# Kernel tuning notes

Measured on AMD Instinct MI355X. Metric: run time of the kernel, lower is better.

The kernel has to match this reference:

```python
import jax, jax.numpy as jnp
import numpy as np

B, N, K, H = 8, 1024, 16, 4
EMB = 1024

def lrelu(x):
    return jnp.where(x >= 0, x, 0.2 * x)

def bn(x, g, b):
    # eval-mode BatchNorm with running_mean=0, running_var=1
    inv = 1.0 / np.sqrt(1.0 + 1e-5)
    shape = (1, -1) + (1,) * (x.ndim - 2)
    return x * (g * inv).reshape(shape) + b.reshape(shape)

def conv1x1(x, w):
    # 1x1 conv == channel matmul; x: (B,C,...), w: (O,C)
    return jnp.einsum('bc...,oc->bo...', x, w)

def knn_idx(x, k):
    # x: (B,C,N); negative squared pairwise distance, top-k largest = nearest
    inner = -2.0 * jnp.einsum('bcn,bcm->bnm', x, x)
    xx = jnp.sum(x * x, axis=1)                      # (B,N)
    pd = -xx[:, :, None] - inner - xx[:, None, :]
    return jax.lax.top_k(pd, k)[1]                   # (B,N,k)

def graph_feature(x, idx):
    b = x.shape[0]
    xt = jnp.transpose(x, (0, 2, 1))                 # (B,N,C)
    nbr = xt[jnp.arange(b)[:, None, None], idx]      # (B,N,K,C) gather
    ctr = jnp.broadcast_to(xt[:, :, None, :], nbr.shape)
    f = jnp.concatenate([nbr - ctr, ctr], axis=-1)   # (B,N,K,2C)
    return jnp.transpose(f, (0, 3, 1, 2))            # (B,2C,N,K)

def mak(x, y, w0, g0, b0, wm, gm, bm, w1, go, bo, ws, gs, bs, out_ch, in_ch):
    # Multi-head adaptive kernel: generate per-point (out,in,H) weights from y, apply to x
    Bc, _, Nc, Kc = x.shape
    y = lrelu(bn(conv1x1(y, w0), g0, b0))
    y = lrelu(bn(conv1x1(y, wm), gm, bm))
    y = conv1x1(y, w1)                               # (B, out*in*H, N, K)
    w = jnp.transpose(y, (0, 2, 3, 1)).reshape(Bc, Nc, Kc, out_ch, in_ch, H)
    xt = jnp.transpose(x, (0, 2, 3, 1))              # (B,N,K,in)
    # per-head matmul then sum over heads == single einsum over i and h
    out = jnp.einsum('bnkoih,bnki->bonk', w, xt)
    out = bn(out, go, bo)
    idt = bn(conv1x1(x, ws), gs, bs)                 # shortcut (in != out)
    return lrelu(out + idt)


def setup_inputs() -> dict:
    ks = jax.random.split(jax.random.key(0), 48)
    it = iter(range(48))
    def nrm(shape, fan):
        return jax.random.normal(ks[next(it)], shape, jnp.float32) / np.sqrt(fan)
    def gam(c):
        return jax.random.uniform(ks[next(it)], (c,), jnp.float32, 0.5, 1.5)
    def bet(c):
        return 0.1 * jax.random.normal(ks[next(it)], (c,), jnp.float32)
    d = {}
    d['x'] = jax.random.normal(ks[next(it)], (B, 3, N), jnp.float32)
    def mak_params(p, feat_c):
        d[p + '_w0'] = nrm((64, feat_c), feat_c); d[p + '_g0'] = gam(64); d[p + '_b0'] = bet(64)
        d[p + '_wm'] = nrm((64, 64), 64); d[p + '_gm'] = gam(64); d[p + '_bm'] = bet(64)
        d[p + '_w1'] = nrm((64 * 6 * H, 64), 64)
        d[p + '_go'] = gam(64); d[p + '_bo'] = bet(64)
        d[p + '_ws'] = nrm((64, 6), 6); d[p + '_gs'] = gam(64); d[p + '_bs'] = bet(64)
    mak_params('m1', 6)
    mak_params('m2', 128)
    d['w3'] = nrm((128, 128), 128); d['g3'] = gam(128); d['b3'] = bet(128)
    d['w4'] = nrm((256, 256), 256); d['g4'] = gam(256); d['b4'] = bet(256)
    d['w5'] = nrm((EMB, 512), 512); d['g5'] = gam(EMB); d['b5'] = bet(EMB)
    d['wl1'] = nrm((512, 2 * EMB), 2 * EMB); d['bn4_g'] = gam(512); d['bn4_b'] = bet(512)
    d['wl2'] = nrm((256, 512), 512); d['bl2'] = bet(256); d['bn5_g'] = gam(256); d['bn5_b'] = bet(256)
    d['wl3'] = nrm((49, 256), 256); d['bl3'] = bet(49)
    return d


def reference(x, m1_w0, m1_g0, m1_b0, m1_wm, m1_gm, m1_bm, m1_w1, m1_go, m1_bo, m1_ws, m1_gs, m1_bs, m2_w0, m2_g0, m2_b0, m2_wm, m2_gm, m2_bm, m2_w1, m2_go, m2_bo, m2_ws, m2_gs, m2_bs, w3, g3, b3, w4, g4, b4, w5, g5, b5, wl1, bn4_g, bn4_b, wl2, bl2, bn5_g, bn5_b, wl3, bl3):
    idx = knn_idx(x, K)                              # common_idx from points
    geo = graph_feature(x, idx)                      # (B,6,N,K); feat_x == geo_x at stage 1
    h = mak(geo, geo, m1_w0, m1_g0, m1_b0, m1_wm, m1_gm, m1_bm, m1_w1, m1_go, m1_bo, m1_ws, m1_gs, m1_bs, 64, 6)
    x1 = h.max(axis=-1)                              # (B,64,N)
    feat2 = graph_feature(x1, idx)                   # (B,128,N,K)
    h = mak(geo, feat2, m2_w0, m2_g0, m2_b0, m2_wm, m2_gm, m2_bm, m2_w1, m2_go, m2_bo, m2_ws, m2_gs, m2_bs, 64, 6)
    x2 = h.max(axis=-1)                              # (B,64,N)
    x3 = lrelu(bn(conv1x1(graph_feature(x2, idx), w3), g3, b3)).max(axis=-1)   # (B,128,N)
    x4 = lrelu(bn(conv1x1(graph_feature(x3, idx), w4), g4, b4)).max(axis=-1)   # (B,256,N)
    xc = jnp.concatenate([x1, x2, x3, x4], axis=1)   # (B,512,N)
    x5 = lrelu(bn(conv1x1(xc, w5), g5, b5))          # (B,EMB,N)
    xp = jnp.concatenate([x5.max(axis=-1), x5.mean(axis=-1)], axis=1)  # (B,2*EMB)
    xf = lrelu(bn(xp @ wl1.T, bn4_g, bn4_b))
    xf = lrelu(bn(xf @ wl2.T + bl2, bn5_g, bn5_b))
    return xf @ wl3.T + bl3                           # (B,49)
```

## Files before the change

kernel.cpp:

```cpp
#include <hip/hip_runtime.h>
#include <math.h>

#define BB 8
#define NN 1024
#define KK 16
#define NKP (NN*KK)
#define BN_INV 0.99999500003749981f

typedef unsigned short u16;
typedef __attribute__((ext_vector_type(8))) short short8;
typedef __attribute__((ext_vector_type(4))) float f32x4;

#define MFMA16(a,b,c) __builtin_amdgcn_mfma_f32_16x16x32_bf16(a,b,c,0,0,0)

__device__ __forceinline__ float lrelu(float v) { return v >= 0.f ? v : 0.2f * v; }

__device__ __forceinline__ u16 f2bf(float f) {
  union { float f; unsigned u; } v; v.f = f;
  unsigned r = v.u + 0x7fff + ((v.u >> 16) & 1);
  return (u16)(r >> 16);
}
__device__ __forceinline__ float bf2f(u16 s) {
  union { unsigned u; float f; } v; v.u = ((unsigned)s) << 16;
  return v.f;
}

constexpr size_t OFF_IDX   = 0;
constexpr size_t OFF_X1P   = 524288;
constexpr size_t OFF_X2P   = 1572864;
constexpr size_t OFF_X3P   = 2621440;
constexpr size_t OFF_MUV   = 2621440;
constexpr size_t OFF_X4P   = 4718592;
constexpr size_t OFF_PMAX  = 8912896;
constexpr size_t OFF_PSUM  = 9437184;
constexpr size_t OFF_XP    = 9961472;
constexpr size_t OFF_XF1   = 10027008;
constexpr size_t OFF_XF2   = 10043392;
constexpr size_t OFF_M1WM  = 10055680;
constexpr size_t OFF_M1W1S = 10063872;
constexpr size_t OFF_M2W0S = 10117120;
constexpr size_t OFF_M2WM  = 10133504;
constexpr size_t OFF_M2W1S = 10141696;
constexpr size_t OFF_W3S   = 10194944;
constexpr size_t OFF_W4S   = 10227712;
constexpr size_t OFF_W5    = 10358784;
constexpr size_t OFF_WL1T  = 11407360;
constexpr size_t OFF_WL2T  = 15601664;
constexpr size_t OFF_WL3T  = 16125952;
constexpr size_t OFF_UV3   = 16177152;
constexpr size_t OFF_UV4   = 20371456;

struct SSeg { const float* w; const float* g; u16* dst; int O; int C; int cpl2; int ch; int stk; int start; };
struct SArgs { SSeg seg[6]; int total; };

__global__ __launch_bounds__(256) void prep_scale_bf16(SArgs a) {
  const int tid = blockIdx.x * 256 + threadIdx.x;
  if (tid >= a.total) return;
  int s = 0;
  #pragma unroll
  for (int i = 1; i < 6; ++i) if (tid >= a.seg[i].start) s = i;
  const SSeg sg = a.seg[s];
  const int e = tid - sg.start;
  const int o2 = e >> sg.cpl2;
  const int c = e & ((1 << sg.cpl2) - 1);
  float v = 0.f;
  if (sg.stk) {
    const int half = sg.O >> 1;
    const int o = o2 & (half - 1);
    const int CIN = 2 * sg.C;
    const float wd = sg.w[o * CIN + c];
    v = (o2 < half) ? wd : (sg.w[o * CIN + sg.C + c] - wd);
    v *= sg.g[o] * BN_INV;
  } else if (c < sg.C) {
    v = sg.w[o2 * sg.C + c];
    if (sg.ch && c >= sg.ch) v -= sg.w[o2 * sg.C + c - sg.ch];
    v *= sg.g[o2] * BN_INV;
  }
  sg.dst[(size_t)(c >> 5) * (sg.O * 32) + o2 * 32 + (c & 31)] = f2bf(v);
}

__global__ __launch_bounds__(256) void prep_w1s_bf16(
    const float* __restrict__ w1a, const float* __restrict__ wsa,
    const float* __restrict__ goa, const float* __restrict__ gsa,
    const float* __restrict__ w1b, const float* __restrict__ wsb,
    const float* __restrict__ gob, const float* __restrict__ gsb,
    u16* __restrict__ dsta, u16* __restrict__ dstb) {
  const int tid = blockIdx.x * 256 + threadIdx.x;
  if (tid >= 64 * 416) return;
  const float* w1 = blockIdx.y ? w1b : w1a;
  const float* wsm = blockIdx.y ? wsb : wsa;
  const float* go = blockIdx.y ? gob : goa;
  const float* gs = blockIdx.y ? gsb : gsa;
  u16* dst = blockIdx.y ? dstb : dsta;
  const int o = tid / 416, ci = tid - o * 416;
  float v = 0.f;
  if (ci < 384) {
    const int ii = ci >> 6, ch = ci & 63;
    const int base = (o * 24 + ii * 4) * 64 + ch;
    v = go[o] * BN_INV * (w1[base] + w1[base + 64] + w1[base + 128] + w1[base + 192]);
  } else if (ci < 390) {
    v = gs[o] * BN_INV * wsm[o * 6 + (ci - 384)];
  }
  dst[(size_t)(ci >> 5) * 2048 + o * 32 + (ci & 31)] = f2bf(v);
}

struct TSeg { const float* w; const float* g; float* dst; int O; int C; int start; };
struct TArgs3 { TSeg seg[3]; int total; };

__global__ __launch_bounds__(256) void prep_transpose_f32(TArgs3 a) {
  const int tid = blockIdx.x * 256 + threadIdx.x;
  if (tid >= a.total) return;
  int s = 0;
  #pragma unroll
  for (int i = 1; i < 3; ++i) if (tid >= a.seg[i].start) s = i;
  const TSeg sg = a.seg[s];
  const int e = tid - sg.start;
  const int c = e / sg.O;
  const int o = e - c * sg.O;
  float v = sg.w[o * sg.C + c];
  if (sg.g) v *= sg.g[o] * BN_INV;
  sg.dst[e] = v;
}

__global__ __launch_bounds__(256) void knn_kernel(const float* __restrict__ x, int* __restrict__ idxout) {
  const int wid  = (blockIdx.x * blockDim.x + threadIdx.x) >> 6;
  const int lane = threadIdx.x & 63;
  const int b = wid >> 10;
  const int n = wid & (NN - 1);
  const float* xb = x + b * 3 * NN;
  const float x0n = xb[n], x1n = xb[NN + n], x2n = xb[2 * NN + n];
  const float xxn = x0n * x0n + x1n * x1n + x2n * x2n;
  float pd[16];
  #pragma unroll
  for (int j = 0; j < 16; ++j) {
    const int m = j * 64 + lane;
    const float x0 = xb[m], x1 = xb[NN + m], x2 = xb[2 * NN + m];
    const float dot = x0n * x0 + x1n * x1 + x2n * x2;
    const float xxm = x0 * x0 + x1 * x1 + x2 * x2;
    pd[j] = 2.f * dot - xxn - xxm;
  }
  for (int r = 0; r < 16; ++r) {
    float bv = pd[0]; int bj = 0;
    #pragma unroll
    for (int j = 1; j < 16; ++j) if (pd[j] > bv) { bv = pd[j]; bj = j; }
    int bm = bj * 64 + lane;
    #pragma unroll
    for (int off = 32; off > 0; off >>= 1) {
      const float ov = __shfl_down(bv, off);
      const int   om = __shfl_down(bm, off);
      if (ov > bv || (ov == bv && om < bm)) { bv = ov; bm = om; }
    }
    bm = __shfl(bm, 0);
    if (lane == 0) idxout[wid * KK + r] = bm;
    const int  cj   = bm >> 6;
    const bool mine = (bm & 63) == lane;
    #pragma unroll
    for (int j = 0; j < 16; ++j) if (mine && j == cj) pd[j] = -INFINITY;
  }
}

__device__ __forceinline__ short8 bfrag64(const u16* T, int pl, int quad, int c0) {
  const int pos = ((c0 >> 3) + quad) ^ (pl & 7);
  return *(const short8*)(T + pl * 64 + pos * 8);
}
__device__ __forceinline__ void writeD64(u16* T, int pl, int quad, const f32x4 a,
                                         const float* __restrict__ bias, int obase) {
  union { ushort4 v; u16 s[4]; } pk;
  #pragma unroll
  for (int r = 0; r < 4; ++r) pk.s[r] = f2bf(lrelu(a[r] + bias[obase + quad * 4 + r]));
  const int g = (obase + quad * 4) >> 3;
  const int pos = g ^ (pl & 7);
  *(ushort4*)(T + pl * 64 + pos * 8 + (quad & 1) * 4) = pk.v;
}

__global__ __launch_bounds__(256) void mak1_uv(
    const float* __restrict__ x, const float* __restrict__ w0,
    const float* __restrict__ g0, const float* __restrict__ b0,
    u16* __restrict__ MUV) {
  const int tid = blockIdx.x * 256 + threadIdx.x;
  if (tid >= BB * NN * 64) return;
  const int o = tid & 63;
  const int p = tid >> 6;
  const int b = p >> 10, n = p & (NN - 1);
  const float* xb = x + b * 3 * NN;
  const float gg = g0[o] * BN_INV;
  float u = 0.f, v = 0.f;
  #pragma unroll
  for (int i = 0; i < 3; ++i) {
    const float wd = w0[o * 6 + i];
    const float wc = w0[o * 6 + 3 + i];
    const float c = xb[i * NN + n];
    u += wd * c;
    v += (wc - wd) * c;
  }
  MUV[(size_t)p * 128 + o]      = f2bf(gg * u);
  MUV[(size_t)p * 128 + 64 + o] = f2bf(gg * v + b0[o]);
}

__global__ __launch_bounds__(256) void mak23_mfma(
    const float* __restrict__ x, const int* __restrict__ idxb, const u16* __restrict__ MUV,
    const u16* __restrict__ wmb, const float* __restrict__ bmv,
    const u16* __restrict__ w1s, const float* __restrict__ bov, const float* __restrict__ bsv,
    u16* __restrict__ Xoutp) {
  __shared__ __align__(16) u16 YMs[4][32 * 64];

  const int t = threadIdx.x;
  const int b = blockIdx.z;
  const int w = t >> 6, l = t & 63;
  const int quad = l >> 4, l15 = l & 15;
  const int cq8 = quad * 8;
  const int p0 = blockIdx.x * 8 + w * 2;
  u16* myYM = YMs[w];
  const float* xb = x + b * 3 * NN;

  int nbr[2];
  #pragma unroll
  for (int pg = 0; pg < 2; ++pg)
    nbr[pg] = idxb[(size_t)(b * NN + p0 + pg) * 16 + l15] & (NN - 1);

  float ge[2][6];
  short8 bgv[2];
  #pragma unroll
  for (int pg = 0; pg < 2; ++pg) {
    const int ctr = p0 + pg;
    union { short8 v; u16 s[8]; } gq;
    gq.v = (short8)(short)0;
    #pragma unroll
    for (int i = 0; i < 3; ++i) {
      const float fc = xb[i * NN + ctr];
      ge[pg][i]     = xb[i * NN + nbr[pg]] - fc;
      ge[pg][3 + i] = fc;
      gq.s[i]     = f2bf(ge[pg][i]);
      gq.s[3 + i] = f2bf(ge[pg][3 + i]);
    }
    bgv[pg] = (quad == 0) ? gq.v : (short8)(short)0;
  }

  short8 bf[2][2];
  #pragma unroll
  for (int pg = 0; pg < 2; ++pg) {
    const u16* urow = MUV + (size_t)(b * NN + nbr[pg]) * 128;
    const u16* vrow = MUV + (size_t)(b * NN + p0 + pg) * 128 + 64;
    #pragma unroll
    for (int kc = 0; kc < 2; ++kc) {
      union { short8 v; u16 s[8]; } uu, vv, rr;
      uu.v = *(const short8*)(urow + kc * 32 + cq8);
      vv.v = *(const short8*)(vrow + kc * 32 + cq8);
      #pragma unroll
      for (int j = 0; j < 8; ++j) rr.s[j] = f2bf(lrelu(bf2f(uu.s[j]) + bf2f(vv.s[j])));
      bf[pg][kc] = rr.v;
    }
  }

  #pragma unroll
  for (int at = 0; at < 4; ++at) {
    f32x4 a2[2];
    #pragma unroll
    for (int pg = 0; pg < 2; ++pg) a2[pg] = (f32x4)0.f;
    #pragma unroll
    for (int kc = 0; kc < 2; ++kc) {
      const short8 af = *(const short8*)(wmb + (size_t)(kc * 64 + at * 16 + l15) * 32 + cq8);
      #pragma unroll
      for (int pg = 0; pg < 2; ++pg) a2[pg] = MFMA16(af, bf[pg][kc], a2[pg]);
    }
    #pragma unroll
    for (int pg = 0; pg < 2; ++pg) writeD64(myYM, pg * 16 + l15, quad, a2[pg], bmv, at * 16);
  }

  short8 bf3[2][2];
  #pragma unroll
  for (int pg = 0; pg < 2; ++pg)
    #pragma unroll
    for (int kc = 0; kc < 2; ++kc)
      bf3[pg][kc] = bfrag64(myYM, pg * 16 + l15, quad, kc * 32);

  f32x4 acc[2][4];
  #pragma unroll
  for (int pg = 0; pg < 2; ++pg)
    #pragma unroll
    for (int at = 0; at < 4; ++at) acc[pg][at] = (f32x4)0.f;

  #pragma unroll
  for (int ii = 0; ii < 6; ++ii) {
    f32x4 tac[2][4];
    #pragma unroll
    for (int pg = 0; pg < 2; ++pg)
      #pragma unroll
      for (int at = 0; at < 4; ++at) tac[pg][at] = (f32x4)0.f;
    #pragma unroll
    for (int kc = 0; kc < 2; ++kc) {
      #pragma unroll
      for (int at = 0; at < 4; ++at) {
        const short8 af = *(const short8*)(w1s + (size_t)((ii * 2 + kc) * 64 + at * 16 + l15) * 32 + cq8);
        #pragma unroll
        for (int pg = 0; pg < 2; ++pg) tac[pg][at] = MFMA16(af, bf3[pg][kc], tac[pg][at]);
      }
    }
    #pragma unroll
    for (int pg = 0; pg < 2; ++pg) {
      const float g = ge[pg][ii];
      #pragma unroll
      for (int at = 0; at < 4; ++at) acc[pg][at] += g * tac[pg][at];
    }
  }
  #pragma unroll
  for (int at = 0; at < 4; ++at) {
    const short8 af = *(const short8*)(w1s + (size_t)(12 * 64 + at * 16 + l15) * 32 + cq8);
    #pragma unroll
    for (int pg = 0; pg < 2; ++pg) acc[pg][at] = MFMA16(af, bgv[pg], acc[pg][at]);
  }

  #pragma unroll
  for (int pg = 0; pg < 2; ++pg) {
    u16* orow = Xoutp + (size_t)(b * NN + p0 + pg) * 64;
    #pragma unroll
    for (int at = 0; at < 4; ++at) {
      union { ushort4 v; u16 s[4]; } pk;
      #pragma unroll
      for (int r = 0; r < 4; ++r) {
        const int o = at * 16 + quad * 4 + r;
        float v = lrelu(acc[pg][at][r] + bov[o] + bsv[o]);
        v = fmaxf(v, __shfl_xor(v, 1));
        v = fmaxf(v, __shfl_xor(v, 2));
        v = fmaxf(v, __shfl_xor(v, 4));
        v = fmaxf(v, __shfl_xor(v, 8));
        pk.s[r] = f2bf(v);
      }
      if (l15 == 0) *(ushort4*)(orow + at * 16 + quad * 4) = pk.v;
    }
  }
}

template<int CH, int COUT2>
__global__ __launch_bounds__(256) void dense_uv(
    const u16* __restrict__ srcp, const u16* __restrict__ w2,
    const float* __restrict__ bias, u16* __restrict__ UV) {
  constexpr int COUT = COUT2 / 2;
  constexpr int NCH = CH / 32;
  const int t = threadIdx.x;
  const int b = blockIdx.z;
  const int w = t >> 6, l = t & 63;
  const int quad = l >> 4, l15 = l & 15;
  const int cq8 = quad * 8;
  int n0, ow0;
  if constexpr (COUT2 >= 256) { n0 = blockIdx.x * 64; ow0 = blockIdx.y * 256 + w * 64; }
  else { n0 = blockIdx.x * 128 + (w >> 1) * 64; ow0 = (w & 1) * 64; }

  f32x4 acc[4][4];
  #pragma unroll
  for (int i = 0; i < 4; ++i)
    #pragma unroll
    for (int j = 0; j < 4; ++j) acc[i][j] = (f32x4)0.f;

  #pragma unroll
  for (int k = 0; k < NCH; ++k) {
    short8 bfr[4];
    #pragma unroll
    for (int pg = 0; pg < 4; ++pg) {
      const int n = n0 + pg * 16 + l15;
      bfr[pg] = *(const short8*)(srcp + (size_t)(b * NN + n) * CH + k * 32 + cq8);
    }
    #pragma unroll
    for (int at = 0; at < 4; ++at) {
      const short8 af = *(const short8*)(w2 + ((size_t)(k * COUT2 + ow0 + at * 16 + l15)) * 32 + cq8);
      #pragma unroll
      for (int pg = 0; pg < 4; ++pg) acc[at][pg] = MFMA16(af, bfr[pg], acc[at][pg]);
    }
  }

  #pragma unroll
  for (int at = 0; at < 4; ++at) {
    const int o0 = ow0 + at * 16 + quad * 4;
    const bool isv = (o0 >= COUT);
    float bb[4];
    #pragma unroll
    for (int r = 0; r < 4; ++r) bb[r] = isv ? bias[o0 + r - COUT] : 0.f;
    #pragma unroll
    for (int pg = 0; pg < 4; ++pg) {
      const int n = n0 + pg * 16 + l15;
      union { ushort4 v; u16 s[4]; } pk;
      #pragma unroll
      for (int r = 0; r < 4; ++r) pk.s[r] = f2bf(acc[at][pg][r] + bb[r]);
      *(ushort4*)(UV + (size_t)(b * NN + n) * COUT2 + o0) = pk.v;
    }
  }
}

__device__ __forceinline__ float4 ubf4(ushort4 q) {
  float4 f;
  f.x = bf2f(q.x); f.y = bf2f(q.y); f.z = bf2f(q.z); f.w = bf2f(q.w);
  return f;
}

template<int COUT>
__global__ __launch_bounds__(256) void gather_max(
    const u16* __restrict__ UV, const int* __restrict__ idxb,
    u16* __restrict__ Xoutp) {
  constexpr int CG = COUT / 4;
  const int tid = blockIdx.x * 256 + threadIdx.x;
  const int cg = tid & (CG - 1);
  const int P = tid / CG;
  const int b = P >> 10;
  const int n = P & (NN - 1);

  const float4 vv = ubf4(*(const ushort4*)(UV + (size_t)P * (2 * COUT) + COUT + 4 * cg));
  const int4* ip = (const int4*)(idxb + (size_t)b * NKP + n * 16);
  float4 m = {-INFINITY, -INFINITY, -INFINITY, -INFINITY};
  #pragma unroll
  for (int kq = 0; kq < 4; ++kq) {
    const int4 iv = ip[kq];
    const int mr[4] = { iv.x & (NN - 1), iv.y & (NN - 1), iv.z & (NN - 1), iv.w & (NN - 1) };
    ushort4 uq[4];
    #pragma unroll
    for (int j = 0; j < 4; ++j)
      uq[j] = *(const ushort4*)(UV + (size_t)(b * NN + mr[j]) * (2 * COUT) + 4 * cg);
    #pragma unroll
    for (int j = 0; j < 4; ++j) {
      const float4 uu = ubf4(uq[j]);
      float4 s;
      s.x = uu.x + vv.x; s.y = uu.y + vv.y; s.z = uu.z + vv.z; s.w = uu.w + vv.w;
      m.x = fmaxf(m.x, fmaxf(s.x, 0.2f * s.x));
      m.y = fmaxf(m.y, fmaxf(s.y, 0.2f * s.y));
      m.z = fmaxf(m.z, fmaxf(s.z, 0.2f * s.z));
      m.w = fmaxf(m.w, fmaxf(s.w, 0.2f * s.w));
    }
  }
  union { ushort4 v; u16 s[4]; } pk;
  pk.s[0] = f2bf(m.x); pk.s[1] = f2bf(m.y); pk.s[2] = f2bf(m.z); pk.s[3] = f2bf(m.w);
  *(ushort4*)(Xoutp + (size_t)P * COUT + 4 * cg) = pk.v;
}

__global__ __launch_bounds__(256) void conv5_mfma(
    const u16* __restrict__ X1P, const u16* __restrict__ X2P,
    const u16* __restrict__ X3P, const u16* __restrict__ X4P,
    const u16* __restrict__ w5b, const float* __restrict__ b5,
    float* __restrict__ PMAX, float* __restrict__ PSUM) {
  const int t = threadIdx.x;
  const int b = blockIdx.z;
  const int n0 = blockIdx.x * 64;
  const int w = t >> 6, l = t & 63;
  const int quad = l >> 4, l15 = l & 15;
  const int cq8 = quad * 8;
  const int ow0 = blockIdx.y * 256 + w * 64;

  f32x4 acc[4][4];
  #pragma unroll
  for (int i = 0; i < 4; ++i)
    #pragma unroll
    for (int j = 0; j < 4; ++j) acc[i][j] = (f32x4)0.f;

  #pragma unroll 4
  for (int k = 0; k < 16; ++k) {
    const int c = k * 32 + cq8;
    short8 bfr[4];
    #pragma unroll
    for (int pg = 0; pg < 4; ++pg) {
      const int n = n0 + pg * 16 + l15;
      const u16* src; int cc;
      if (c < 64)       { src = X1P + (size_t)(b * NN + n) * 64;  cc = c; }
      else if (c < 128) { src = X2P + (size_t)(b * NN + n) * 64;  cc = c - 64; }
      else if (c < 256) { src = X3P + (size_t)(b * NN + n) * 128; cc = c - 128; }
      else              { src = X4P + (size_t)(b * NN + n) * 256; cc = c - 256; }
      bfr[pg] = *(const short8*)(src + cc);
    }
    #pragma unroll
    for (int at = 0; at < 4; ++at) {
      const short8 af = *(const short8*)(w5b + ((size_t)(k * 1024 + ow0 + at * 16 + l15)) * 32 + cq8);
      #pragma unroll
      for (int pg = 0; pg < 4; ++pg) acc[at][pg] = MFMA16(af, bfr[pg], acc[at][pg]);
    }
  }

  #pragma unroll
  for (int at = 0; at < 4; ++at) {
    f32x4 pmx, psm;
    #pragma unroll
    for (int r = 0; r < 4; ++r) {
      const float bb = b5[ow0 + at * 16 + quad * 4 + r];
      float m = -INFINITY, s = 0.f;
      #pragma unroll
      for (int pg = 0; pg < 4; ++pg) {
        const float v = lrelu(acc[at][pg][r] + bb);
        m = fmaxf(m, v); s += v;
      }
      #pragma unroll
      for (int msk = 1; msk < 16; msk <<= 1) {
        m = fmaxf(m, __shfl_xor(m, msk));
        s += __shfl_xor(s, msk);
      }
      pmx[r] = m; psm[r] = s;
    }
    if (l15 == 0) {
      float* dm = PMAX + (size_t)(b * 16 + blockIdx.x) * 1024 + ow0 + at * 16 + quad * 4;
      float* ds = PSUM + (size_t)(b * 16 + blockIdx.x) * 1024 + ow0 + at * 16 + quad * 4;
      *(f32x4*)dm = pmx;
      *(f32x4*)ds = psm;
    }
  }
}

__global__ __launch_bounds__(256) void reduce5(const float* __restrict__ PMAX, const float* __restrict__ PSUM,
                                               float* __restrict__ XPg) {
  const int tid = blockIdx.x * 256 + threadIdx.x;
  const int b = tid >> 10, o = tid & 1023;
  float m = -INFINITY, s = 0.f;
  for (int pt = 0; pt < 16; ++pt) {
    m = fmaxf(m, PMAX[(size_t)(b * 16 + pt) * 1024 + o]);
    s += PSUM[(size_t)(b * 16 + pt) * 1024 + o];
  }
  XPg[b * 2048 + o] = m;
  XPg[b * 2048 + 1024 + o] = s * (1.f / 1024.f);
}

__global__ __launch_bounds__(256) void fc1_kernel(const float* __restrict__ XPg, const float* __restrict__ wl1t,
                                                  const float* __restrict__ bn4_b, float* __restrict__ XF1) {
  __shared__ float red[64 * 5];
  const int t = threadIdx.x;
  const int b = blockIdx.y;
  const int o = blockIdx.x * 64 + (t & 63);
  const int cq = t >> 6;
  const float* xp = XPg + b * 2048;
  float acc = 0.f;
  for (int c = cq * 512; c < cq * 512 + 512; ++c) acc = fmaf(wl1t[c * 512 + o], xp[c], acc);
  red[(t & 63) * 5 + cq] = acc;
  __syncthreads();
  if (t < 64) {
    const int oo = blockIdx.x * 64 + t;
    const float v = red[t * 5] + red[t * 5 + 1] + red[t * 5 + 2] + red[t * 5 + 3] + bn4_b[oo];
    XF1[b * 512 + oo] = lrelu(v);
  }
}

__global__ __launch_bounds__(256) void fc2_kernel(const float* __restrict__ XF1, const float* __restrict__ wl2t,
                                                  const float* __restrict__ bl2, const float* __restrict__ bn5_g,
                                                  const float* __restrict__ bn5_b, float* __restrict__ XF2) {
  __shared__ float red[64 * 5];
  const int t = threadIdx.x;
  const int b = blockIdx.y;
  const int o = blockIdx.x * 64 + (t & 63);
  const int cq = t >> 6;
  const float* xf = XF1 + b * 512;
  float acc = 0.f;
  for (int c = cq * 128; c < cq * 128 + 128; ++c) acc = fmaf(wl2t[c * 256 + o], xf[c], acc);
  red[(t & 63) * 5 + cq] = acc;
  __syncthreads();
  if (t < 64) {
    const int oo = blockIdx.x * 64 + t;
    const float bias = bl2[oo] * (bn5_g[oo] * BN_INV) + bn5_b[oo];
    const float v = red[t * 5] + red[t * 5 + 1] + red[t * 5 + 2] + red[t * 5 + 3] + bias;
    XF2[b * 256 + oo] = lrelu(v);
  }
}

__global__ __launch_bounds__(256) void fc3_kernel(const float* __restrict__ XF2, const float* __restrict__ wl3t,
                                                  const float* __restrict__ bl3, float* __restrict__ out) {
  __shared__ float red[64 * 5];
  const int t = threadIdx.x;
  const int b = blockIdx.y;
  const int ol = t & 63;
  const int cq = t >> 6;
  const float* xf = XF2 + b * 256;
  float acc = 0.f;
  if (ol < 49) for (int c = cq * 64; c < cq * 64 + 64; ++c) acc = fmaf(wl3t[c * 49 + ol], xf[c], acc);
  red[ol * 5 + cq] = acc;
  __syncthreads();
  if (t < 49) out[b * 49 + t] = red[t * 5] + red[t * 5 + 1] + red[t * 5 + 2] + red[t * 5 + 3] + bl3[t];
}

extern "C" void kernel_launch(void* const* d_in, const int* in_sizes, int n_in,
                              void* d_out, int out_size, void* d_ws, size_t ws_size,
                              hipStream_t stream) {
  (void)in_sizes; (void)n_in; (void)out_size; (void)ws_size;
  const float* x     = (const float*)d_in[0];
  const float* m1_w0 = (const float*)d_in[1];
  const float* m1_g0 = (const float*)d_in[2];
  const float* m1_b0 = (const float*)d_in[3];
  const float* m1_wm = (const float*)d_in[4];
  const float* m1_gm = (const float*)d_in[5];
  const float* m1_bm = (const float*)d_in[6];
  const float* m1_w1 = (const float*)d_in[7];
  const float* m1_go = (const float*)d_in[8];
  const float* m1_bo = (const float*)d_in[9];
  const float* m1_ws = (const float*)d_in[10];
  const float* m1_gs = (const float*)d_in[11];
  const float* m1_bs = (const float*)d_in[12];
  const float* m2_w0 = (const float*)d_in[13];
  const float* m2_g0 = (const float*)d_in[14];
  const float* m2_b0 = (const float*)d_in[15];
  const float* m2_wm = (const float*)d_in[16];
  const float* m2_gm = (const float*)d_in[17];
  const float* m2_bm = (const float*)d_in[18];
  const float* m2_w1 = (const float*)d_in[19];
  const float* m2_go = (const float*)d_in[20];
  const float* m2_bo = (const float*)d_in[21];
  const float* m2_ws = (const float*)d_in[22];
  const float* m2_gs = (const float*)d_in[23];
  const float* m2_bs = (const float*)d_in[24];
  const float* w3    = (const float*)d_in[25];
  const float* g3    = (const float*)d_in[26];
  const float* b3    = (const float*)d_in[27];
  const float* w4    = (const float*)d_in[28];
  const float* g4    = (const float*)d_in[29];
  const float* b4    = (const float*)d_in[30];
  const float* w5    = (const float*)d_in[31];
  const float* g5    = (const float*)d_in[32];
  const float* b5    = (const float*)d_in[33];
  const float* wl1   = (const float*)d_in[34];
  const float* bn4_g = (const float*)d_in[35];
  const float* bn4_b = (const float*)d_in[36];
  const float* wl2   = (const float*)d_in[37];
  const float* bl2   = (const float*)d_in[38];
  const float* bn5_g = (const float*)d_in[39];
  const float* bn5_b = (const float*)d_in[40];
  const float* wl3   = (const float*)d_in[41];
  const float* bl3   = (const float*)d_in[42];

  char* wsb = (char*)d_ws;
  int*  IDX  = (int*)(wsb + OFF_IDX);
  u16*  X1P  = (u16*)(wsb + OFF_X1P);
  u16*  X2P  = (u16*)(wsb + OFF_X2P);
  u16*  X3P  = (u16*)(wsb + OFF_X3P);
  u16*  X4P  = (u16*)(wsb + OFF_X4P);
  u16*  MUV  = (u16*)(wsb + OFF_MUV);
  float* PMAX = (float*)(wsb + OFF_PMAX);
  float* PSUM = (float*)(wsb + OFF_PSUM);
  float* XPg  = (float*)(wsb + OFF_XP);
  float* XF1  = (float*)(wsb + OFF_XF1);
  float* XF2  = (float*)(wsb + OFF_XF2);
  u16*  M1WM = (u16*)(wsb + OFF_M1WM);
  u16*  M1W1S = (u16*)(wsb + OFF_M1W1S);
  u16*  M2W0S = (u16*)(wsb + OFF_M2W0S);
  u16*  M2WM = (u16*)(wsb + OFF_M2WM);
  u16*  M2W1S = (u16*)(wsb + OFF_M2W1S);
  u16*  W3S  = (u16*)(wsb + OFF_W3S);
  u16*  W4S  = (u16*)(wsb + OFF_W4S);
  u16*  W5B  = (u16*)(wsb + OFF_W5);
  float* WL1T = (float*)(wsb + OFF_WL1T);
  float* WL2T = (float*)(wsb + OFF_WL2T);
  float* WL3T = (float*)(wsb + OFF_WL3T);
  u16*  UV3  = (u16*)(wsb + OFF_UV3);
  u16*  UV4  = (u16*)(wsb + OFF_UV4);

  SArgs sa; int st = 0;
  auto sset = [&](int i, const float* w, const float* g, u16* dst, int O, int C, int cpl2, int ch, int stk) {
    sa.seg[i].w = w; sa.seg[i].g = g; sa.seg[i].dst = dst; sa.seg[i].O = O; sa.seg[i].C = C;
    sa.seg[i].cpl2 = cpl2; sa.seg[i].ch = ch; sa.seg[i].stk = stk; sa.seg[i].start = st;
    st += O << cpl2;
  };
  sset(0, m1_wm, m1_gm, M1WM, 64, 64, 6, 0, 0);
  sset(1, m2_w0, m2_g0, M2W0S, 128, 64, 6, 0, 1);
  sset(2, m2_wm, m2_gm, M2WM, 64, 64, 6, 0, 0);
  sset(3, w3, g3, W3S, 256, 64, 6, 0, 1);
  sset(4, w4, g4, W4S, 512, 128, 7, 0, 1);
  sset(5, w5, g5, W5B, 1024, 512, 9, 0, 0);
  sa.total = st;

  TArgs3 ta; int tt = 0;
  auto tset = [&](int i, const float* w, const float* g, float* dst, int O, int C) {
    ta.seg[i].w = w; ta.seg[i].g = g; ta.seg[i].dst = dst; ta.seg[i].O = O; ta.seg[i].C = C;
    ta.seg[i].start = tt; tt += O * C;
  };
  tset(0, wl1, bn4_g, WL1T, 512, 2048);
  tset(1, wl2, bn5_g, WL2T, 256, 512);
  tset(2, wl3, nullptr, WL3T, 49, 256);
  ta.total = tt;

  hipLaunchKernelGGL(prep_scale_bf16, dim3((sa.total + 255) / 256), dim3(256), 0, stream, sa);
  hipLaunchKernelGGL(prep_w1s_bf16, dim3(104, 2), dim3(256), 0, stream,
                     m1_w1, m1_ws, m1_go, m1_gs, m2_w1, m2_ws, m2_go, m2_gs, M1W1S, M2W1S);
  hipLaunchKernelGGL(prep_transpose_f32, dim3((ta.total + 255) / 256), dim3(256), 0, stream, ta);

  hipLaunchKernelGGL(knn_kernel, dim3(2048), dim3(256), 0, stream, x, IDX);

  hipLaunchKernelGGL(mak1_uv, dim3((BB * NN * 64 + 255) / 256), dim3(256), 0, stream,
                     x, m1_w0, m1_g0, m1_b0, MUV);
  hipLaunchKernelGGL(mak23_mfma, dim3(128, 1, BB), dim3(256), 0, stream,
                     x, IDX, MUV, M1WM, m1_bm, M1W1S, m1_bo, m1_bs, X1P);

  hipLaunchKernelGGL((dense_uv<64, 128>), dim3(8, 1, BB), dim3(256), 0, stream, X1P, M2W0S, m2_b0, MUV);
  hipLaunchKernelGGL(mak23_mfma, dim3(128, 1, BB), dim3(256), 0, stream,
                     x, IDX, MUV, M2WM, m2_bm, M2W1S, m2_bo, m2_bs, X2P);

  hipLaunchKernelGGL((dense_uv<64, 256>), dim3(16, 1, BB), dim3(256), 0, stream, X2P, W3S, b3, UV3);
  hipLaunchKernelGGL((gather_max<128>), dim3(1024), dim3(256), 0, stream, UV3, IDX, X3P);
  hipLaunchKernelGGL((dense_uv<128, 512>), dim3(16, 2, BB), dim3(256), 0, stream, X3P, W4S, b4, UV4);
  hipLaunchKernelGGL((gather_max<256>), dim3(2048), dim3(256), 0, stream, UV4, IDX, X4P);

  hipLaunchKernelGGL(conv5_mfma, dim3(16, 4, BB), dim3(256), 0, stream,
                     X1P, X2P, X3P, X4P, W5B, b5, PMAX, PSUM);
  hipLaunchKernelGGL(reduce5, dim3(32), dim3(256), 0, stream, PMAX, PSUM, XPg);

  hipLaunchKernelGGL(fc1_kernel, dim3(8, BB), dim3(256), 0, stream, XPg, WL1T, bn4_b, XF1);
  hipLaunchKernelGGL(fc2_kernel, dim3(4, BB), dim3(256), 0, stream, XF1, WL2T, bl2, bn5_g, bn5_b, XF2);
  hipLaunchKernelGGL(fc3_kernel, dim3(1, BB), dim3(256), 0, stream, XF2, WL3T, bl3, (float*)d_out);
}
```

Baseline: 388.9 us.

## Merge prep, knn/uv, reduce and FC kernels to cut launch count

Combines the three weight-prep kernels into one launch and puts the knn and mak1_uv work into a single grid that branches on block index. It also folds the max/mean reduction into fc1, which each block now recomputes into shared memory, and fuses fc2 and fc3 into one kernel per batch. The aim is fewer kernel launches and inter-kernel gaps. The cost is redundant reduction work in fc1 and less parallelism for fc2, which now uses one block per batch.

Result: no change. 388.5 us (-0.1%).

```diff
diff --git a/kernel.cpp b/kernel.cpp
--- a/kernel.cpp
+++ b/kernel.cpp
@@ -33,9 +33,7 @@
 constexpr size_t OFF_X4P   = 4718592;
 constexpr size_t OFF_PMAX  = 8912896;
 constexpr size_t OFF_PSUM  = 9437184;
-constexpr size_t OFF_XP    = 9961472;
 constexpr size_t OFF_XF1   = 10027008;
-constexpr size_t OFF_XF2   = 10043392;
 constexpr size_t OFF_M1WM  = 10055680;
 constexpr size_t OFF_M1W1S = 10063872;
 constexpr size_t OFF_M2W0S = 10117120;
@@ -52,110 +50,136 @@
 
 struct SSeg { const float* w; const float* g; u16* dst; int O; int C; int cpl2; int ch; int stk; int start; };
 struct SArgs { SSeg seg[6]; int total; };
-
-__global__ __launch_bounds__(256) void prep_scale_bf16(SArgs a) {
-  const int tid = blockIdx.x * 256 + threadIdx.x;
-  if (tid >= a.total) return;
-  int s = 0;
-  #pragma unroll
-  for (int i = 1; i < 6; ++i) if (tid >= a.seg[i].start) s = i;
-  const SSeg sg = a.seg[s];
-  const int e = tid - sg.start;
-  const int o2 = e >> sg.cpl2;
-  const int c = e & ((1 << sg.cpl2) - 1);
-  float v = 0.f;
-  if (sg.stk) {
-    const int half = sg.O >> 1;
-    const int o = o2 & (half - 1);
-    const int CIN = 2 * sg.C;
-    const float wd = sg.w[o * CIN + c];
-    v = (o2 < half) ? wd : (sg.w[o * CIN + sg.C + c] - wd);
-    v *= sg.g[o] * BN_INV;
-  } else if (c < sg.C) {
-    v = sg.w[o2 * sg.C + c];
-    if (sg.ch && c >= sg.ch) v -= sg.w[o2 * sg.C + c - sg.ch];
-    v *= sg.g[o2] * BN_INV;
-  }
-  sg.dst[(size_t)(c >> 5) * (sg.O * 32) + o2 * 32 + (c & 31)] = f2bf(v);
-}
-
-__global__ __launch_bounds__(256) void prep_w1s_bf16(
-    const float* __restrict__ w1a, const float* __restrict__ wsa,
-    const float* __restrict__ goa, const float* __restrict__ gsa,
-    const float* __restrict__ w1b, const float* __restrict__ wsb,
-    const float* __restrict__ gob, const float* __restrict__ gsb,
-    u16* __restrict__ dsta, u16* __restrict__ dstb) {
-  const int tid = blockIdx.x * 256 + threadIdx.x;
-  if (tid >= 64 * 416) return;
-  const float* w1 = blockIdx.y ? w1b : w1a;
-  const float* wsm = blockIdx.y ? wsb : wsa;
-  const float* go = blockIdx.y ? gob : goa;
-  const float* gs = blockIdx.y ? gsb : gsa;
-  u16* dst = blockIdx.y ? dstb : dsta;
-  const int o = tid / 416, ci = tid - o * 416;
-  float v = 0.f;
-  if (ci < 384) {
-    const int ii = ci >> 6, ch = ci & 63;
-    const int base = (o * 24 + ii * 4) * 64 + ch;
-    v = go[o] * BN_INV * (w1[base] + w1[base + 64] + w1[base + 128] + w1[base + 192]);
-  } else if (ci < 390) {
-    v = gs[o] * BN_INV * wsm[o * 6 + (ci - 384)];
-  }
-  dst[(size_t)(ci >> 5) * 2048 + o * 32 + (ci & 31)] = f2bf(v);
-}
-
 struct TSeg { const float* w; const float* g; float* dst; int O; int C; int start; };
 struct TArgs3 { TSeg seg[3]; int total; };
-
-__global__ __launch_bounds__(256) void prep_transpose_f32(TArgs3 a) {
-  const int tid = blockIdx.x * 256 + threadIdx.x;
-  if (tid >= a.total) return;
-  int s = 0;
-  #pragma unroll
-  for (int i = 1; i < 3; ++i) if (tid >= a.seg[i].start) s = i;
-  const TSeg sg = a.seg[s];
-  const int e = tid - sg.start;
-  const int c = e / sg.O;
-  const int o = e - c * sg.O;
-  float v = sg.w[o * sg.C + c];
-  if (sg.g) v *= sg.g[o] * BN_INV;
-  sg.dst[e] = v;
-}
-
-__global__ __launch_bounds__(256) void knn_kernel(const float* __restrict__ x, int* __restrict__ idxout) {
-  const int wid  = (blockIdx.x * blockDim.x + threadIdx.x) >> 6;
-  const int lane = threadIdx.x & 63;
-  const int b = wid >> 10;
-  const int n = wid & (NN - 1);
-  const float* xb = x + b * 3 * NN;
-  const float x0n = xb[n], x1n = xb[NN + n], x2n = xb[2 * NN + n];
-  const float xxn = x0n * x0n + x1n * x1n + x2n * x2n;
-  float pd[16];
-  #pragma unroll
-  for (int j = 0; j < 16; ++j) {
-    const int m = j * 64 + lane;
-    const float x0 = xb[m], x1 = xb[NN + m], x2 = xb[2 * NN + m];
-    const float dot = x0n * x0 + x1n * x1 + x2n * x2;
-    const float xxm = x0 * x0 + x1 * x1 + x2 * x2;
-    pd[j] = 2.f * dot - xxn - xxm;
-  }
-  for (int r = 0; r < 16; ++r) {
-    float bv = pd[0]; int bj = 0;
-    #pragma unroll
-    for (int j = 1; j < 16; ++j) if (pd[j] > bv) { bv = pd[j]; bj = j; }
-    int bm = bj * 64 + lane;
-    #pragma unroll
-    for (int off = 32; off > 0; off >>= 1) {
-      const float ov = __shfl_down(bv, off);
-      const int   om = __shfl_down(bm, off);
-      if (ov > bv || (ov == bv && om < bm)) { bv = ov; bm = om; }
-    }
-    bm = __shfl(bm, 0);
-    if (lane == 0) idxout[wid * KK + r] = bm;
-    const int  cj   = bm >> 6;
-    const bool mine = (bm & 63) == lane;
-    #pragma unroll
-    for (int j = 0; j < 16; ++j) if (mine && j == cj) pd[j] = -INFINITY;
+struct PrepAll {
+  SArgs sa;
+  const float *w1a, *wsa, *goa, *gsa, *w1b, *wsb, *gob, *gsb;
+  u16 *dsta, *dstb;
+  TArgs3 ta;
+  int nA, nB;
+};
+
+__global__ __launch_bounds__(256) void prep_all(PrepAll P) {
+  const int bx = blockIdx.x;
+  const int t = threadIdx.x;
+  if (bx < P.nA) {
+    const int tid = bx * 256 + t;
+    if (tid >= P.sa.total) return;
+    int s = 0;
+    #pragma unroll
+    for (int i = 1; i < 6; ++i) if (tid >= P.sa.seg[i].start) s = i;
+    const SSeg sg = P.sa.seg[s];
+    const int e = tid - sg.start;
+    const int o2 = e >> sg.cpl2;
+    const int c = e & ((1 << sg.cpl2) - 1);
+    float v = 0.f;
+    if (sg.stk) {
+      const int half = sg.O >> 1;
+      const int o = o2 & (half - 1);
+      const int CIN = 2 * sg.C;
+      const float wd = sg.w[o * CIN + c];
+      v = (o2 < half) ? wd : (sg.w[o * CIN + sg.C + c] - wd);
+      v *= sg.g[o] * BN_INV;
+    } else if (c < sg.C) {
+      v = sg.w[o2 * sg.C + c];
+      if (sg.ch && c >= sg.ch) v -= sg.w[o2 * sg.C + c - sg.ch];
+      v *= sg.g[o2] * BN_INV;
+    }
+    sg.dst[(size_t)(c >> 5) * (sg.O * 32) + o2 * 32 + (c & 31)] = f2bf(v);
+  } else if (bx < P.nA + P.nB) {
+    const int tid = (bx - P.nA) * 256 + t;
+    const int set = (tid >= 26624) ? 1 : 0;
+    const int id2 = tid - set * 26624;
+    const float* w1 = set ? P.w1b : P.w1a;
+    const float* wsm = set ? P.wsb : P.wsa;
+    const float* go = set ? P.gob : P.goa;
+    const float* gs = set ? P.gsb : P.gsa;
+    u16* dst = set ? P.dstb : P.dsta;
+    const int o = id2 / 416, ci = id2 - o * 416;
+    float v = 0.f;
+    if (ci < 384) {
+      const int ii = ci >> 6, ch = ci & 63;
+      const int base = (o * 24 + ii * 4) * 64 + ch;
+      v = go[o] * BN_INV * (w1[base] + w1[base + 64] + w1[base + 128] + w1[base + 192]);
+    } else if (ci < 390) {
+      v = gs[o] * BN_INV * wsm[o * 6 + (ci - 384)];
+    }
+    dst[(size_t)(ci >> 5) * 2048 + o * 32 + (ci & 31)] = f2bf(v);
+  } else {
+    const int tid = (bx - P.nA - P.nB) * 256 + t;
+    if (tid >= P.ta.total) return;
+    int s = 0;
+    #pragma unroll
+    for (int i = 1; i < 3; ++i) if (tid >= P.ta.seg[i].start) s = i;
+    const TSeg sg = P.ta.seg[s];
+    const int e = tid - sg.start;
+    const int c = e / sg.O;
+    const int o = e - c * sg.O;
+    float v = sg.w[o * sg.C + c];
+    if (sg.g) v *= sg.g[o] * BN_INV;
+    sg.dst[e] = v;
+  }
+}
+
+__global__ __launch_bounds__(256) void knn_mak1uv(
+    const float* __restrict__ x, int* __restrict__ idxout,
+    const float* __restrict__ w0, const float* __restrict__ g0,
+    const float* __restrict__ b0, u16* __restrict__ MUV) {
+  if (blockIdx.x < 2048) {
+    const int wid  = (blockIdx.x * blockDim.x + threadIdx.x) >> 6;
+    const int lane = threadIdx.x & 63;
+    const int b = wid >> 10;
+    const int n = wid & (NN - 1);
+    const float* xb = x + b * 3 * NN;
+    const float x0n = xb[n], x1n = xb[NN + n], x2n = xb[2 * NN + n];
+    const float xxn = x0n * x0n + x1n * x1n + x2n * x2n;
+    float pd[16];
+    #pragma unroll
+    for (int j = 0; j < 16; ++j) {
+      const int m = j * 64 + lane;
+      const float x0 = xb[m], x1 = xb[NN + m], x2 = xb[2 * NN + m];
+      const float dot = x0n * x0 + x1n * x1 + x2n * x2;
+      const float xxm = x0 * x0 + x1 * x1 + x2 * x2;
+      pd[j] = 2.f * dot - xxn - xxm;
+    }
+    for (int r = 0; r < 16; ++r) {
+      float bv = pd[0]; int bj = 0;
+      #pragma unroll
+      for (int j = 1; j < 16; ++j) if (pd[j] > bv) { bv = pd[j]; bj = j; }
+      int bm = bj * 64 + lane;
+      #pragma unroll
+      for (int off = 32; off > 0; off >>= 1) {
+        const float ov = __shfl_down(bv, off);
+        const int   om = __shfl_down(bm, off);
+        if (ov > bv || (ov == bv && om < bm)) { bv = ov; bm = om; }
+      }
+      bm = __shfl(bm, 0);
+      if (lane == 0) idxout[wid * KK + r] = bm;
+      const int  cj   = bm >> 6;
+      const bool mine = (bm & 63) == lane;
+      #pragma unroll
+      for (int j = 0; j < 16; ++j) if (mine && j == cj) pd[j] = -INFINITY;
+    }
+  } else {
+    const int tid = (blockIdx.x - 2048) * 256 + threadIdx.x;
+    if (tid >= BB * NN * 64) return;
+    const int o = tid & 63;
+    const int p = tid >> 6;
+    const int b = p >> 10, n = p & (NN - 1);
+    const float* xb = x + b * 3 * NN;
+    const float gg = g0[o] * BN_INV;
+    float u = 0.f, v = 0.f;
+    #pragma unroll
+    for (int i = 0; i < 3; ++i) {
+      const float wd = w0[o * 6 + i];
+      const float wc = w0[o * 6 + 3 + i];
+      const float c = xb[i * NN + n];
+      u += wd * c;
+      v += (wc - wd) * c;
+    }
+    MUV[(size_t)p * 128 + o]      = f2bf(gg * u);
+    MUV[(size_t)p * 128 + 64 + o] = f2bf(gg * v + b0[o]);
   }
 }
 
@@ -171,30 +195,6 @@
   const int g = (obase + quad * 4) >> 3;
   const int pos = g ^ (pl & 7);
   *(ushort4*)(T + pl * 64 + pos * 8 + (quad & 1) * 4) = pk.v;
-}
-
-__global__ __launch_bounds__(256) void mak1_uv(
-    const float* __restrict__ x, const float* __restrict__ w0,
-    const float* __restrict__ g0, const float* __restrict__ b0,
-    u16* __restrict__ MUV) {
-  const int tid = blockIdx.x * 256 + threadIdx.x;
-  if (tid >= BB * NN * 64) return;
-  const int o = tid & 63;
-  const int p = tid >> 6;
-  const int b = p >> 10, n = p & (NN - 1);
-  const float* xb = x + b * 3 * NN;
-  const float gg = g0[o] * BN_INV;
-  float u = 0.f, v = 0.f;
-  #pragma unroll
-  for (int i = 0; i < 3; ++i) {
-    const float wd = w0[o * 6 + i];
-    const float wc = w0[o * 6 + 3 + i];
-    const float c = xb[i * NN + n];
-    u += wd * c;
-    v += (wc - wd) * c;
-  }
-  MUV[(size_t)p * 128 + o]      = f2bf(gg * u);
-  MUV[(size_t)p * 128 + 64 + o] = f2bf(gg * v + b0[o]);
 }
 
 __global__ __launch_bounds__(256) void mak23_mfma(
@@ -499,27 +499,27 @@
   }
 }
 
-__global__ __launch_bounds__(256) void reduce5(const float* __restrict__ PMAX, const float* __restrict__ PSUM,
-                                               float* __restrict__ XPg) {
-  const int tid = blockIdx.x * 256 + threadIdx.x;
-  const int b = tid >> 10, o = tid & 1023;
-  float m = -INFINITY, s = 0.f;
-  for (int pt = 0; pt < 16; ++pt) {
-    m = fmaxf(m, PMAX[(size_t)(b * 16 + pt) * 1024 + o]);
-    s += PSUM[(size_t)(b * 16 + pt) * 1024 + o];
-  }
-  XPg[b * 2048 + o] = m;
-  XPg[b * 2048 + 1024 + o] = s * (1.f / 1024.f);
-}
-
-__global__ __launch_bounds__(256) void fc1_kernel(const float* __restrict__ XPg, const float* __restrict__ wl1t,
-                                                  const float* __restrict__ bn4_b, float* __restrict__ XF1) {
+__global__ __launch_bounds__(256) void fc1_kernel(
+    const float* __restrict__ PMAX, const float* __restrict__ PSUM,
+    const float* __restrict__ wl1t, const float* __restrict__ bn4_b,
+    float* __restrict__ XF1) {
+  __shared__ float xp[2048];
   __shared__ float red[64 * 5];
   const int t = threadIdx.x;
   const int b = blockIdx.y;
+  for (int e = t; e < 1024; e += 256) {
+    float m = -INFINITY, s = 0.f;
+    #pragma unroll 4
+    for (int pt = 0; pt < 16; ++pt) {
+      m = fmaxf(m, PMAX[(size_t)(b * 16 + pt) * 1024 + e]);
+      s += PSUM[(size_t)(b * 16 + pt) * 1024 + e];
+    }
+    xp[e] = m;
+    xp[1024 + e] = s * (1.f / 1024.f);
+  }
+  __syncthreads();
   const int o = blockIdx.x * 64 + (t & 63);
   const int cq = t >> 6;
-  const float* xp = XPg + b * 2048;
   float acc = 0.f;
   for (int c = cq * 512; c < cq * 512 + 512; ++c) acc = fmaf(wl1t[c * 512 + o], xp[c], acc);
   red[(t & 63) * 5 + cq] = acc;
@@ -531,40 +531,31 @@
   }
 }
 
-__global__ __launch_bounds__(256) void fc2_kernel(const float* __restrict__ XF1, const float* __restrict__ wl2t,
-                                                  const float* __restrict__ bl2, const float* __restrict__ bn5_g,
-                                                  const float* __restrict__ bn5_b, float* __restrict__ XF2) {
-  __shared__ float red[64 * 5];
+__global__ __launch_bounds__(256) void fc23_kernel(
+    const float* __restrict__ XF1, const float* __restrict__ wl2t,
+    const float* __restrict__ bl2, const float* __restrict__ bn5_g,
+    const float* __restrict__ bn5_b, const float* __restrict__ wl3t,
+    const float* __restrict__ bl3, float* __restrict__ out) {
+  __shared__ float xf1s[512];
+  __shared__ float xf2s[256];
   const int t = threadIdx.x;
-  const int b = blockIdx.y;
-  const int o = blockIdx.x * 64 + (t & 63);
-  const int cq = t >> 6;
-  const float* xf = XF1 + b * 512;
-  float acc = 0.f;
-  for (int c = cq * 128; c < cq * 128 + 128; ++c) acc = fmaf(wl2t[c * 256 + o], xf[c], acc);
-  red[(t & 63) * 5 + cq] = acc;
+  const int b = blockIdx.x;
+  for (int e = t; e < 512; e += 256) xf1s[e] = XF1[b * 512 + e];
   __syncthreads();
-  if (t < 64) {
-    const int oo = blockIdx.x * 64 + t;
-    const float bias = bl2[oo] * (bn5_g[oo] * BN_INV) + bn5_b[oo];
-    const float v = red[t * 5] + red[t * 5 + 1] + red[t * 5 + 2] + red[t * 5 + 3] + bias;
-    XF2[b * 256 + oo] = lrelu(v);
-  }
-}
-
-__global__ __launch_bounds__(256) void fc3_kernel(const float* __restrict__ XF2, const float* __restrict__ wl3t,
-                                                  const float* __restrict__ bl3, float* __restrict__ out) {
-  __shared__ float red[64 * 5];
-  const int t = threadIdx.x;
-  const int b = blockIdx.y;
-  const int ol = t & 63;
-  const int cq = t >> 6;
-  const float* xf = XF2 + b * 256;
-  float acc = 0.f;
-  if (ol < 49) for (int c = cq * 64; c < cq * 64 + 64; ++c) acc = fmaf(wl3t[c * 49 + ol], xf[c], acc);
-  red[ol * 5 + cq] = acc;
+  {
+    float acc = 0.f;
+    #pragma unroll 8
+    for (int c = 0; c < 512; ++c) acc = fmaf(wl2t[c * 256 + t], xf1s[c], acc);
+    const float bias = bl2[t] * (bn5_g[t] * BN_INV) + bn5_b[t];
+    xf2s[t] = lrelu(acc + bias);
+  }
   __syncthreads();
-  if (t < 49) out[b * 49 + t] = red[t * 5] + red[t * 5 + 1] + red[t * 5 + 2] + red[t * 5 + 3] + bl3[t];
+  if (t < 49) {
+    float acc = 0.f;
+    #pragma unroll 8
+    for (int c = 0; c < 256; ++c) acc = fmaf(wl3t[c * 49 + t], xf2s[c], acc);
+    out[b * 49 + t] = acc + bl3[t];
+  }
 }
 
 extern "C" void kernel_launch(void* const* d_in, const int* in_sizes, int n_in,
@@ -624,9 +615,7 @@
   u16*  MUV  = (u16*)(wsb + OFF_MUV);
   float* PMAX = (float*)(wsb + OFF_PMAX);
   float* PSUM = (float*)(wsb + OFF_PSUM);
-  float* XPg  = (float*)(wsb + OFF_XP);
   float* XF1  = (float*)(wsb + OFF_XF1);
-  float* XF2  = (float*)(wsb + OFF_XF2);
   u16*  M1WM = (u16*)(wsb + OFF_M1WM);
   u16*  M1W1S = (u16*)(wsb + OFF_M1W1S);
   u16*  M2W0S = (u16*)(wsb + OFF_M2W0S);
@@ -641,10 +630,11 @@
   u16*  UV3  = (u16*)(wsb + OFF_UV3);
   u16*  UV4  = (u16*)(wsb + OFF_UV4);
 
-  SArgs sa; int st = 0;
+  PrepAll P;
+  int st = 0;
   auto sset = [&](int i, const float* w, const float* g, u16* dst, int O, int C, int cpl2, int ch, int stk) {
-    sa.seg[i].w = w; sa.seg[i].g = g; sa.seg[i].dst = dst; sa.seg[i].O = O; sa.seg[i].C = C;
-    sa.seg[i].cpl2 = cpl2; sa.seg[i].ch = ch; sa.seg[i].stk = stk; sa.seg[i].start = st;
+    P.sa.seg[i].w = w; P.sa.seg[i].g = g; P.sa.seg[i].dst = dst; P.sa.seg[i].O = O; P.sa.seg[i].C = C;
+    P.sa.seg[i].cpl2 = cpl2; P.sa.seg[i].ch = ch; P.sa.seg[i].stk = stk; P.sa.seg[i].start = st;
     st += O << cpl2;
   };
   sset(0, m1_wm, m1_gm, M1WM, 64, 64, 6, 0, 0);
@@ -653,27 +643,31 @@
   sset(3, w3, g3, W3S, 256, 64, 6, 0, 1);
   sset(4, w4, g4, W4S, 512, 128, 7, 0, 1);
   sset(5, w5, g5, W5B, 1024, 512, 9, 0, 0);
-  sa.total = st;
-
-  TArgs3 ta; int tt = 0;
+  P.sa.total = st;
+
+  P.w1a = m1_w1; P.wsa = m1_ws; P.goa = m1_go; P.gsa = m1_gs;
+  P.w1b = m2_w1; P.wsb = m2_ws; P.gob = m2_go; P.gsb = m2_gs;
+  P.dsta = M1W1S; P.dstb = M2W1S;
+
+  int tt = 0;
   auto tset = [&](int i, const float* w, const float* g, float* dst, int O, int C) {
-    ta.seg[i].w = w; ta.seg[i].g = g; ta.seg[i].dst = dst; ta.seg[i].O = O; ta.seg[i].C = C;
-    ta.seg[i].start = tt; tt += O * C;
+    P.ta.seg[i].w = w; P.ta.seg[i].g = g; P.ta.seg[i].dst = dst; P.ta.seg[i].O = O; P.ta.seg[i].C = C;
+    P.ta.seg[i].start = tt; tt += O * C;
   };
   tset(0, wl1, bn4_g, WL1T, 512, 2048);
   tset(1, wl2, bn5_g, WL2T, 256, 512);
   tset(2, wl3, nullptr, WL3T, 49, 256);
-  ta.total = tt;
-
-  hipLaunchKernelGGL(prep_scale_bf16, dim3((sa.total + 255) / 256), dim3(256), 0, stream, sa);
-  hipLaunchKernelGGL(prep_w1s_bf16, dim3(104, 2), dim3(256), 0, stream,
-                     m1_w1, m1_ws, m1_go, m1_gs, m2_w1, m2_ws, m2_go, m2_gs, M1W1S, M2W1S);
-  hipLaunchKernelGGL(prep_transpose_f32, dim3((ta.total + 255) / 256), dim3(256), 0, stream, ta);
-
-  hipLaunchKernelGGL(knn_kernel, dim3(2048), dim3(256), 0, stream, x, IDX);
-
-  hipLaunchKernelGGL(mak1_uv, dim3((BB * NN * 64 + 255) / 256), dim3(256), 0, stream,
-                     x, m1_w0, m1_g0, m1_b0, MUV);
+  P.ta.total = tt;
+
+  P.nA = (P.sa.total + 255) / 256;
+  P.nB = (2 * 64 * 416 + 255) / 256;
+  const int nC = (P.ta.total + 255) / 256;
+
+  hipLaunchKernelGGL(prep_all, dim3(P.nA + P.nB + nC), dim3(256), 0, stream, P);
+
+  hipLaunchKernelGGL(knn_mak1uv, dim3(4096), dim3(256), 0, stream,
+                     x, IDX, m1_w0, m1_g0, m1_b0, MUV);
+
   hipLaunchKernelGGL(mak23_mfma, dim3(128, 1, BB), dim3(256), 0, stream,
                      x, IDX, MUV, M1WM, m1_bm, M1W1S, m1_bo, m1_bs, X1P);
 
@@ -688,9 +682,8 @@
 
   hipLaunchKernelGGL(conv5_mfma, dim3(16, 4, BB), dim3(256), 0, stream,
                      X1P, X2P, X3P, X4P, W5B, b5, PMAX, PSUM);
-  hipLaunchKernelGGL(reduce5, dim3(32), dim3(256), 0, stream, PMAX, PSUM, XPg);
-
-  hipLaunchKernelGGL(fc1_kernel, dim3(8, BB), dim3(256), 0, stream, XPg, WL1T, bn4_b, XF1);
-  hipLaunchKernelGGL(fc2_kernel, dim3(4, BB), dim3(256), 0, stream, XF1, WL2T, bl2, bn5_g, bn5_b, XF2);
-  hipLaunchKernelGGL(fc3_kernel, dim3(1, BB), dim3(256), 0, stream, XF2, WL3T, bl3, (float*)d_out);
-}
+
+  hipLaunchKernelGGL(fc1_kernel, dim3(8, BB), dim3(256), 0, stream, PMAX, PSUM, WL1T, bn4_b, XF1);
+  hipLaunchKernelGGL(fc23_kernel, dim3(BB), dim3(256), 0, stream,
+                     XF1, WL2T, bl2, bn5_g, bn5_b, WL3T, bl3, (float*)d_out);
+}
```
